# Optimization experiments

Measured on AMD Instinct MI355X. Metric: run time of the kernel, lower is better.

The kernel has to match this reference:

```python
import jax, jax.numpy as jnp
import numpy as np

BATCH, SEQ, IN, HID = 8192, 512, 5, 64


def setup_inputs() -> dict:
    key = jax.random.key(0)
    ks = jax.random.split(key, 7)
    s_ih = 1.0 / np.sqrt(HID)
    return {
        "inputs": jax.random.normal(ks[0], (BATCH, SEQ, IN), dtype=jnp.float32),
        "W_ih": jax.random.uniform(ks[1], (4 * HID, IN), minval=-s_ih, maxval=s_ih, dtype=jnp.float32),
        "W_hh": jax.random.uniform(ks[2], (4 * HID, HID), minval=-s_ih, maxval=s_ih, dtype=jnp.float32),
        "b_ih": jax.random.uniform(ks[3], (4 * HID,), minval=-s_ih, maxval=s_ih, dtype=jnp.float32),
        "b_hh": jax.random.uniform(ks[4], (4 * HID,), minval=-s_ih, maxval=s_ih, dtype=jnp.float32),
        "fc_w": jax.random.uniform(ks[5], (1, HID), minval=-s_ih, maxval=s_ih, dtype=jnp.float32),
        "fc_b": jax.random.uniform(ks[6], (1,), minval=-s_ih, maxval=s_ih, dtype=jnp.float32),
    }


def reference(inputs, W_ih, W_hh, b_ih, b_hh, fc_w, fc_b):
    B = inputs.shape[0]
    # Precompute input projections for all timesteps: [S, B, 4H]
    x_proj = jnp.einsum('bsi,gi->sbg', inputs, W_ih) + b_ih + b_hh

    def step(carry, xg):
        hx, cx = carry
        gates = xg + hx @ W_hh.T  # [B, 4H]
        i, f, g, o = jnp.split(gates, 4, axis=-1)  # PyTorch LSTMCell gate order
        i = jax.nn.sigmoid(i)
        f = jax.nn.sigmoid(f)
        g = jnp.tanh(g)
        o = jax.nn.sigmoid(o)
        cx = f * cx + i * g
        hx = o * jnp.tanh(cx)
        return (hx, cx), None

    h0 = jnp.zeros((B, HID), dtype=inputs.dtype)
    c0 = jnp.zeros((B, HID), dtype=inputs.dtype)
    (hx, _), _ = jax.lax.scan(step, (h0, c0), x_proj)
    pred = hx @ fc_w.T + fc_b  # [B, 1]
    return jax.nn.leaky_relu(pred, negative_slope=0.01)
```

## Files before the change

kernel.cpp:

```cpp
#include <hip/hip_runtime.h>

#define BATCH 8192
#define SEQ 512
#define INND 5
#define HID 64
#define STRIDE 104

typedef __attribute__((ext_vector_type(8))) short short8;
typedef __attribute__((ext_vector_type(4))) float f32x4;
typedef __attribute__((ext_vector_type(2))) float f32x2;

__device__ __forceinline__ unsigned short f2bf(float f) {
  union { float f; unsigned u; } v; v.f = f;
  unsigned r = v.u + 0x7FFFu + ((v.u >> 16) & 1u);
  return (unsigned short)(r >> 16);
}
__device__ __forceinline__ float bf2f(unsigned short s) {
  union { unsigned u; float f; } v; v.u = ((unsigned)s) << 16;
  return v.f;
}
#define RCP(x) __builtin_amdgcn_rcpf(x)

__global__ __launch_bounds__(256) void lstm_kernel(
    const float* __restrict__ inputs, const float* __restrict__ W_ih,
    const float* __restrict__ W_hh, const float* __restrict__ b_ih,
    const float* __restrict__ b_hh, const float* __restrict__ fc_w,
    const float* __restrict__ fc_b, float* __restrict__ out) {
  __shared__ unsigned short hbuf[2][16][STRIDE] __attribute__((aligned(16)));

  const int tid = threadIdx.x;
  const int lane = tid & 63;
  const int w = tid >> 6;
  const int l15 = lane & 15;
  const int kg = lane >> 4;
  const int l7 = l15 & 7;
  const int b0 = blockIdx.x * 16;

  short8 wf[4][3];
#pragma unroll
  for (int X = 0; X < 4; ++X) {
    const float sc = (X == 2) ? -2.f : -1.f;
    const int col = 64 * X + 16 * w + l15;
    const float* wr = W_hh + col * 64;
#pragma unroll
    for (int s = 0; s < 2; ++s) {
      const float* p = wr + 32 * s + 8 * kg;
      short8 v;
#pragma unroll
      for (int j = 0; j < 8; ++j) v[j] = (short)f2bf(sc * p[j]);
      wf[X][s] = v;
    }
    short8 e;
#pragma unroll
    for (int j = 0; j < 8; ++j) e[j] = 0;
    if (kg == 0) {
#pragma unroll
      for (int j = 0; j < 5; ++j) e[j] = (short)f2bf(sc * W_ih[col * 5 + j]);
      e[5] = (short)f2bf(sc * (b_ih[col] + b_hh[col]));
    }
    wf[X][2] = e;
  }

  unsigned short* const hb0 = &hbuf[0][0][0];
  const int rd0 = l15 * STRIDE + ((kg ^ l7) << 3);
  const int rd1 = l15 * STRIDE + (((4 | kg) ^ l7) << 3);
  const int rd2 = l15 * STRIDE + 64 + ((kg ^ (l15 & 3)) << 3);
  const int hwr = l15 * STRIDE + (((w << 4) | (kg << 2)) ^ (l7 << 3));

  const bool writer = (tid < 16 * INND);
  const int wrow = tid / INND;
  const int wi = tid - wrow * INND;
  const float* xptr = inputs + (size_t)(b0 + wrow) * (SEQ * INND) + wi;
  const int xcol = 64 + (wi | ((wrow & 3) << 3));

  for (int i = tid; i < 2 * 16 * STRIDE; i += 256) hb0[i] = 0;
  __syncthreads();
  if (tid < 32) {
    const int r = tid & 15;
    hbuf[tid >> 4][r][64 + (5 | ((r & 3) << 3))] = 0x3F80;
  }
  float x_next = 0.f;
  if (writer) {
    hbuf[0][wrow][xcol] = f2bf(xptr[0]);
    x_next = xptr[INND];
  }
  __syncthreads();

  f32x2 cst[2] = {{0.f, 0.f}, {0.f, 0.f}};
  for (int t = 0; t < SEQ; ++t) {
    const int cur = t & 1, nxt = cur ^ 1;

    float x_n2 = 0.f;
    if (writer && t + 2 < SEQ) x_n2 = xptr[(t + 2) * INND];

    const unsigned short* hc = hb0 + cur * (16 * STRIDE);
    f32x4 acc0 = {0.f, 0.f, 0.f, 0.f};
    f32x4 acc1 = {0.f, 0.f, 0.f, 0.f};
    f32x4 acc2 = {0.f, 0.f, 0.f, 0.f};
    f32x4 acc3 = {0.f, 0.f, 0.f, 0.f};
    {
      const short8 a0 = *(const short8*)(hc + rd0);
      acc0 = __builtin_amdgcn_mfma_f32_16x16x32_bf16(wf[0][0], a0, acc0, 0, 0, 0);
      acc1 = __builtin_amdgcn_mfma_f32_16x16x32_bf16(wf[1][0], a0, acc1, 0, 0, 0);
      acc2 = __builtin_amdgcn_mfma_f32_16x16x32_bf16(wf[2][0], a0, acc2, 0, 0, 0);
      acc3 = __builtin_amdgcn_mfma_f32_16x16x32_bf16(wf[3][0], a0, acc3, 0, 0, 0);
      const short8 a1 = *(const short8*)(hc + rd1);
      acc0 = __builtin_amdgcn_mfma_f32_16x16x32_bf16(wf[0][1], a1, acc0, 0, 0, 0);
      acc1 = __builtin_amdgcn_mfma_f32_16x16x32_bf16(wf[1][1], a1, acc1, 0, 0, 0);
      acc2 = __builtin_amdgcn_mfma_f32_16x16x32_bf16(wf[2][1], a1, acc2, 0, 0, 0);
      acc3 = __builtin_amdgcn_mfma_f32_16x16x32_bf16(wf[3][1], a1, acc3, 0, 0, 0);
      const short8 a2 = *(const short8*)(hc + rd2);
      acc0 = __builtin_amdgcn_mfma_f32_16x16x32_bf16(wf[0][2], a2, acc0, 0, 0, 0);
      acc1 = __builtin_amdgcn_mfma_f32_16x16x32_bf16(wf[1][2], a2, acc1, 0, 0, 0);
      acc2 = __builtin_amdgcn_mfma_f32_16x16x32_bf16(wf[2][2], a2, acc2, 0, 0, 0);
      acc3 = __builtin_amdgcn_mfma_f32_16x16x32_bf16(wf[3][2], a2, acc3, 0, 0, 0);
    }

    unsigned pk[2];
#pragma unroll
    for (int p = 0; p < 2; ++p) {
      f32x2 ti = {acc0[2 * p], acc0[2 * p + 1]};
      f32x2 tf = {acc1[2 * p], acc1[2 * p + 1]};
      f32x2 tg = {acc2[2 * p], acc2[2 * p + 1]};
      f32x2 to = {acc3[2 * p], acc3[2 * p + 1]};
      ti.x = fminf(ti.x, 17.f); ti.y = fminf(ti.y, 17.f);
      tf.x = fminf(tf.x, 17.f); tf.y = fminf(tf.y, 17.f);
      tg.x = fminf(tg.x, 34.f); tg.y = fminf(tg.y, 34.f);
      to.x = fminf(to.x, 17.f); to.y = fminf(to.y, 17.f);
      f32x2 Ei, Ef, Eg, Eo;
      Ei.x = __expf(ti.x); Ei.y = __expf(ti.y);
      Ef.x = __expf(tf.x); Ef.y = __expf(tf.y);
      Eg.x = __expf(tg.x); Eg.y = __expf(tg.y);
      Eo.x = __expf(to.x); Eo.y = __expf(to.y);
      const f32x2 ai = Ei + 1.f, af = Ef + 1.f, ag = Eg + 1.f, ao = Eo + 1.f;
      const f32x2 u = ai * ag, v = af * ao;
      const f32x2 P = u * v;
      f32x2 r; r.x = RCP(P.x); r.y = RCP(P.y);
      const f32x2 rv = r * v;
      const f32x2 ru = r * u;
      const f32x2 Pig = (1.f - Eg) * rv;
      const f32x2 sf = ru * ao;
      const f32x2 so = ru * af;
      const f32x2 c = sf * cst[p] + Pig;
      cst[p] = c;
      f32x2 tc;
      tc.x = fminf(-2.f * c.x, 80.f); tc.y = fminf(-2.f * c.y, 80.f);
      f32x2 Ec; Ec.x = __expf(tc.x); Ec.y = __expf(tc.y);
      const f32x2 ac = Ec + 1.f;
      f32x2 rc; rc.x = RCP(ac.x); rc.y = RCP(ac.y);
      const f32x2 th = (1.f - Ec) * rc;
      const f32x2 h = so * th;
      pk[p] = ((unsigned)f2bf(h.x)) | (((unsigned)f2bf(h.y)) << 16);
    }
    {
      uint2 pkv; pkv.x = pk[0]; pkv.y = pk[1];
      *(uint2*)(hb0 + nxt * (16 * STRIDE) + hwr) = pkv;
    }
    if (writer && t + 1 < SEQ) hbuf[nxt][wrow][xcol] = f2bf(x_next);
    x_next = x_n2;
    __syncthreads();
  }

  if (tid < 64) {
    const int row = tid >> 2, seg = tid & 3;
    const int key = (row & 7) << 3;
    float sum = 0.f;
#pragma unroll
    for (int j = 0; j < 16; ++j)
      sum += bf2f(hbuf[0][row][(seg * 16 + j) ^ key]) * fc_w[seg * 16 + j];
    sum += __shfl_xor(sum, 1);
    sum += __shfl_xor(sum, 2);
    if (seg == 0) {
      const float p = sum + fc_b[0];
      out[b0 + row] = p > 0.f ? p : 0.01f * p;
    }
  }
}

extern "C" void kernel_launch(void* const* d_in, const int* in_sizes, int n_in,
                              void* d_out, int out_size, void* d_ws, size_t ws_size,
                              hipStream_t stream) {
  const float* inputs = (const float*)d_in[0];
  const float* W_ih = (const float*)d_in[1];
  const float* W_hh = (const float*)d_in[2];
  const float* b_ih = (const float*)d_in[3];
  const float* b_hh = (const float*)d_in[4];
  const float* fc_w = (const float*)d_in[5];
  const float* fc_b = (const float*)d_in[6];
  float* out = (float*)d_out;

  lstm_kernel<<<BATCH / 16, 256, 0, stream>>>(inputs, W_ih, W_hh, b_ih, b_hh,
                                              fc_w, fc_b, out);
}
```

Baseline: 559.3 us.

## Fold log2e into weights, use exp2, drop clamps, hardware bf16 pack, unswizzle LDS

Pre-scales the recurrent and input weights by log2(e) so gate activations use the native exp2 instruction without a multiply. It drops most pre-exp clamps, reformulates tanh(g) and tanh(c) as 2*sigmoid-1, and packs h with the v_cvt_pk_bf16_f32 instruction instead of manual rounding. It also removes the XOR swizzle from the LDS hidden-state layout for simpler addressing, which may add bank conflicts. Removing the clamps risks inf/NaN on large pre-activations.

```diff
diff --git a/kernel.cpp b/kernel.cpp
--- a/kernel.cpp
+++ b/kernel.cpp
@@ -20,6 +20,8 @@
   return v.f;
 }
 #define RCP(x) __builtin_amdgcn_rcpf(x)
+#define EXP2(x) __builtin_amdgcn_exp2f(x)
+#define NL2E 1.44269504088896340736f
 
 __global__ __launch_bounds__(256) void lstm_kernel(
     const float* __restrict__ inputs, const float* __restrict__ W_ih,
@@ -33,13 +35,12 @@
   const int w = tid >> 6;
   const int l15 = lane & 15;
   const int kg = lane >> 4;
-  const int l7 = l15 & 7;
   const int b0 = blockIdx.x * 16;
 
   short8 wf[4][3];
 #pragma unroll
   for (int X = 0; X < 4; ++X) {
-    const float sc = (X == 2) ? -2.f : -1.f;
+    const float sc = (X == 2) ? (-2.f * NL2E) : (-NL2E);
     const int col = 64 * X + 16 * w + l15;
     const float* wr = W_hh + col * 64;
 #pragma unroll
@@ -62,23 +63,20 @@
   }
 
   unsigned short* const hb0 = &hbuf[0][0][0];
-  const int rd0 = l15 * STRIDE + ((kg ^ l7) << 3);
-  const int rd1 = l15 * STRIDE + (((4 | kg) ^ l7) << 3);
-  const int rd2 = l15 * STRIDE + 64 + ((kg ^ (l15 & 3)) << 3);
-  const int hwr = l15 * STRIDE + (((w << 4) | (kg << 2)) ^ (l7 << 3));
+  const int rd0 = l15 * STRIDE + 8 * kg;
+  const int rd1 = rd0 + 32;
+  const int rd2 = rd0 + 64;
+  const int hwr = l15 * STRIDE + 16 * w + 4 * kg;
 
   const bool writer = (tid < 16 * INND);
   const int wrow = tid / INND;
   const int wi = tid - wrow * INND;
   const float* xptr = inputs + (size_t)(b0 + wrow) * (SEQ * INND) + wi;
-  const int xcol = 64 + (wi | ((wrow & 3) << 3));
+  const int xcol = 64 + wi;
 
   for (int i = tid; i < 2 * 16 * STRIDE; i += 256) hb0[i] = 0;
   __syncthreads();
-  if (tid < 32) {
-    const int r = tid & 15;
-    hbuf[tid >> 4][r][64 + (5 | ((r & 3) << 3))] = 0x3F80;
-  }
+  if (tid < 32) hbuf[tid >> 4][tid & 15][69] = 0x3F80;
   float x_next = 0.f;
   if (writer) {
     hbuf[0][wrow][xcol] = f2bf(xptr[0]);
@@ -88,12 +86,12 @@
 
   f32x2 cst[2] = {{0.f, 0.f}, {0.f, 0.f}};
   for (int t = 0; t < SEQ; ++t) {
-    const int cur = t & 1, nxt = cur ^ 1;
+    const int nxt = (t & 1) ^ 1;
 
     float x_n2 = 0.f;
     if (writer && t + 2 < SEQ) x_n2 = xptr[(t + 2) * INND];
 
-    const unsigned short* hc = hb0 + cur * (16 * STRIDE);
+    const unsigned short* hc = hb0 + (t & 1) * (16 * STRIDE);
     f32x4 acc0 = {0.f, 0.f, 0.f, 0.f};
     f32x4 acc1 = {0.f, 0.f, 0.f, 0.f};
     f32x4 acc2 = {0.f, 0.f, 0.f, 0.f};
@@ -119,38 +117,32 @@
     unsigned pk[2];
 #pragma unroll
     for (int p = 0; p < 2; ++p) {
-      f32x2 ti = {acc0[2 * p], acc0[2 * p + 1]};
-      f32x2 tf = {acc1[2 * p], acc1[2 * p + 1]};
-      f32x2 tg = {acc2[2 * p], acc2[2 * p + 1]};
-      f32x2 to = {acc3[2 * p], acc3[2 * p + 1]};
-      ti.x = fminf(ti.x, 17.f); ti.y = fminf(ti.y, 17.f);
-      tf.x = fminf(tf.x, 17.f); tf.y = fminf(tf.y, 17.f);
-      tg.x = fminf(tg.x, 34.f); tg.y = fminf(tg.y, 34.f);
-      to.x = fminf(to.x, 17.f); to.y = fminf(to.y, 17.f);
       f32x2 Ei, Ef, Eg, Eo;
-      Ei.x = __expf(ti.x); Ei.y = __expf(ti.y);
-      Ef.x = __expf(tf.x); Ef.y = __expf(tf.y);
-      Eg.x = __expf(tg.x); Eg.y = __expf(tg.y);
-      Eo.x = __expf(to.x); Eo.y = __expf(to.y);
+      Ei.x = EXP2(acc0[2 * p]); Ei.y = EXP2(acc0[2 * p + 1]);
+      Ef.x = EXP2(acc1[2 * p]); Ef.y = EXP2(acc1[2 * p + 1]);
+      Eg.x = EXP2(acc2[2 * p]); Eg.y = EXP2(acc2[2 * p + 1]);
+      Eo.x = EXP2(acc3[2 * p]); Eo.y = EXP2(acc3[2 * p + 1]);
       const f32x2 ai = Ei + 1.f, af = Ef + 1.f, ag = Eg + 1.f, ao = Eo + 1.f;
-      const f32x2 u = ai * ag, v = af * ao;
-      const f32x2 P = u * v;
+      const f32x2 u = ai * ag, vv = af * ao;
+      const f32x2 P = u * vv;
       f32x2 r; r.x = RCP(P.x); r.y = RCP(P.y);
-      const f32x2 rv = r * v;
+      const f32x2 rv = r * vv;
       const f32x2 ru = r * u;
-      const f32x2 Pig = (1.f - Eg) * rv;
+      const f32x2 si = rv * ag;
+      const f32x2 sg2 = rv * ai;
       const f32x2 sf = ru * ao;
       const f32x2 so = ru * af;
-      const f32x2 c = sf * cst[p] + Pig;
+      const f32x2 tg = 2.f * sg2 - 1.f;
+      const f32x2 c = sf * cst[p] + si * tg;
       cst[p] = c;
-      f32x2 tc;
-      tc.x = fminf(-2.f * c.x, 80.f); tc.y = fminf(-2.f * c.y, 80.f);
-      f32x2 Ec; Ec.x = __expf(tc.x); Ec.y = __expf(tc.y);
+      f32x2 tc = c * (-2.f * NL2E);
+      tc.x = fminf(tc.x, 49.f); tc.y = fminf(tc.y, 49.f);
+      f32x2 Ec; Ec.x = EXP2(tc.x); Ec.y = EXP2(tc.y);
       const f32x2 ac = Ec + 1.f;
       f32x2 rc; rc.x = RCP(ac.x); rc.y = RCP(ac.y);
-      const f32x2 th = (1.f - Ec) * rc;
+      const f32x2 th = 2.f * rc - 1.f;
       const f32x2 h = so * th;
-      pk[p] = ((unsigned)f2bf(h.x)) | (((unsigned)f2bf(h.y)) << 16);
+      asm("v_cvt_pk_bf16_f32 %0, %1, %2" : "=v"(pk[p]) : "v"(h.x), "v"(h.y));
     }
     {
       uint2 pkv; pkv.x = pk[0]; pkv.y = pk[1];
@@ -163,11 +155,10 @@
 
   if (tid < 64) {
     const int row = tid >> 2, seg = tid & 3;
-    const int key = (row & 7) << 3;
     float sum = 0.f;
 #pragma unroll
     for (int j = 0; j < 16; ++j)
-      sum += bf2f(hbuf[0][row][(seg * 16 + j) ^ key]) * fc_w[seg * 16 + j];
+      sum += bf2f(hbuf[0][row][seg * 16 + j]) * fc_w[seg * 16 + j];
     sum += __shfl_xor(sum, 1);
     sum += __shfl_xor(sum, 2);
     if (seg == 0) {
```

After: 470.0 us. 1.19x faster.
